# Kernel tuning notes

Hardware: AMD Instinct MI355X
Metric: run time of the kernel (lower is better)

## Reference

```python
import jax, jax.numpy as jnp
import numpy as np

H = 128  # GRU units


def _gru_dir(x, W, U, b, reverse):
    """Keras GRU (reset_after=True, gate order z,r,h). x: [B,T,D].
    Returns (final_state [B,H], all_states [B,T,H])."""
    b_i, b_h = b[0], b[1]  # input bias, recurrent bias, each [3H]
    # Precompute input projections for all timesteps: [T,B,3H]
    xp = jnp.einsum('btd,dh->tbh', x, W) + b_i

    def step(h, xt):
        rec = h @ U + b_h                       # [B,3H]
        xz, xr, xh = jnp.split(xt, 3, axis=-1)
        rz, rr, rh = jnp.split(rec, 3, axis=-1)
        z = jax.nn.sigmoid(xz + rz)
        r = jax.nn.sigmoid(xr + rr)
        hh = jnp.tanh(xh + r * rh)
        hn = z * h + (1.0 - z) * hh
        return hn, hn

    h0 = jnp.zeros((x.shape[0], H), x.dtype)
    hT, hs = jax.lax.scan(step, h0, xp, reverse=reverse)
    return hT, jnp.transpose(hs, (1, 0, 2))  # [B,T,H]


def _forward(x, Ws, Us, bs, Wd, bd):
    out = x
    for l in range(3):
        fT, f = _gru_dir(out, Ws[l, 0], Us[l, 0], bs[l, 0], reverse=False)
        bT, b = _gru_dir(out, Ws[l, 1], Us[l, 1], bs[l, 1], reverse=True)
        if l < 2:  # return_sequences=True, concat merge
            out = jnp.concatenate([f, b], axis=-1)      # [B,T,2H]
        else:      # return_sequences=False: final states
            out = jnp.concatenate([fT, bT], axis=-1)    # [B,2H]
    return jax.nn.sigmoid(out @ Wd + bd)                # [B,1]


def setup_inputs() -> dict:
    key = jax.random.key(0)
    ks = jax.random.split(key, 5)
    B, T, D = 256, 512, 256
    x = jax.random.normal(ks[0], (B, T, D), jnp.float32)
    # glorot-ish scaling to keep gates in a sane range
    Ws = jax.random.normal(ks[1], (3, 2, D, 3 * H), jnp.float32) * (1.0 / np.sqrt(D))
    Us = jax.random.normal(ks[2], (3, 2, H, 3 * H), jnp.float32) * (1.0 / np.sqrt(H))
    bs = jnp.zeros((3, 2, 2, 3 * H), jnp.float32)
    Wd = jax.random.normal(ks[3], (2 * H, 1), jnp.float32) * (1.0 / np.sqrt(2 * H))
    bd = jnp.zeros((1,), jnp.float32)
    return {"x": x, "Ws": Ws, "Us": Us, "bs": bs, "Wd": Wd, "bd": bd}


def reference(x, Ws, Us, bs, Wd, bd):
    return _forward(x, Ws, Us, bs, Wd, bd)
```

## Files before the change

kernel.cpp:

```cpp
#include <hip/hip_runtime.h>
#include <hip/hip_bf16.h>

#define DEV __device__ __forceinline__

constexpr int B_ = 256;
constexpr int T_ = 512;
constexpr int H_ = 128;
constexpr int K_ = 256;
constexpr int G_ = 384;
constexpr int M_ = B_ * T_;

using bf16 = __hip_bfloat16;
typedef short bf16x8 __attribute__((ext_vector_type(8)));
typedef float f32x4 __attribute__((ext_vector_type(4)));
typedef float f32x2 __attribute__((ext_vector_type(2)));

DEV float tof(float x) { return x; }
DEV float tof(bf16 x) { return __bfloat162float(x); }
DEV void stor(float* p, float v) { *p = v; }
DEV void stor(bf16* p, float v) { *p = __float2bfloat16(v); }

DEV unsigned short f2bs(float f) {
  union { float f; unsigned u; } v;
  v.f = f;
  unsigned r = (v.u + 0x7FFFu + ((v.u >> 16) & 1u)) >> 16;
  return (unsigned short)r;
}
DEV float bs2f(unsigned short s) {
  union { unsigned u; float f; } v;
  v.u = ((unsigned)s) << 16;
  return v.f;
}

DEV float fsigmoid(float x) {
  return __builtin_amdgcn_rcpf(1.f + __expf(-x));
}
DEV float ftanh(float x) {
  x = fminf(20.f, fmaxf(-20.f, x));
  float e = __expf(-2.f * x);
  return (1.f - e) * __builtin_amdgcn_rcpf(1.f + e);
}

DEV void barrier_lds() {
  asm volatile("s_waitcnt lgkmcnt(0)\n\ts_barrier" ::: "memory");
}

DEV void pin4(float4& v) {
  asm volatile("" : "+v"(v.x), "+v"(v.y), "+v"(v.z), "+v"(v.w));
}

DEV f32x4 mfma16(bf16x8 a, bf16x8 b, f32x4 c) {
  return __builtin_amdgcn_mfma_f32_16x16x32_bf16(a, b, c, 0, 0, 0);
}

DEV void gload16(const ushort* g, ushort* l) {
  __builtin_amdgcn_global_load_lds(
      (const __attribute__((address_space(1))) void*)g,
      (__attribute__((address_space(3))) void*)l, 16, 0, 0);
}

DEV float dppx1(float x) {
  return __int_as_float(
      __builtin_amdgcn_update_dpp(0, __float_as_int(x), 0xB1, 0xF, 0xF, true));
}
DEV float dppx2(float x) {
  return __int_as_float(
      __builtin_amdgcn_update_dpp(0, __float_as_int(x), 0x4E, 0xF, 0xF, true));
}
DEV float dppx7(float x) {
  return __int_as_float(
      __builtin_amdgcn_update_dpp(0, __float_as_int(x), 0x141, 0xF, 0xF, true));
}

__global__ __launch_bounds__(256) void convX_kernel(
    const float* __restrict__ x, ushort* __restrict__ hiA,
    ushort* __restrict__ loA) {
  const int n4 = M_ * K_ / 4;
  for (int idx = blockIdx.x * blockDim.x + threadIdx.x; idx < n4;
       idx += gridDim.x * blockDim.x) {
    float4 v = ((const float4*)x)[idx];
    ushort4 h, l;
    h.x = f2bs(v.x); l.x = f2bs(v.x - bs2f(h.x));
    h.y = f2bs(v.y); l.y = f2bs(v.y - bs2f(h.y));
    h.z = f2bs(v.z); l.z = f2bs(v.z - bs2f(h.z));
    h.w = f2bs(v.w); l.w = f2bs(v.w - bs2f(h.w));
    ((ushort4*)hiA)[idx] = h;
    ((ushort4*)loA)[idx] = l;
  }
}

__global__ __launch_bounds__(256) void convW_kernel(
    const float* __restrict__ W, ushort* __restrict__ WhiT,
    ushort* __restrict__ WloT) {
  const int ncol = blockIdx.x;
  const int dir = ncol / G_, j = ncol % G_;
  const int k = threadIdx.x;
  const float f = W[((size_t)dir * K_ + k) * G_ + j];
  const unsigned short hi = f2bs(f);
  WhiT[(size_t)ncol * K_ + k] = hi;
  WloT[(size_t)ncol * K_ + k] = f2bs(f - bs2f(hi));
}

template <typename XT>
__global__ __launch_bounds__(256, 2) void gemm3_kernel(
    const ushort* __restrict__ Ahi, const ushort* __restrict__ Alo,
    const ushort* __restrict__ WhiT, const ushort* __restrict__ WloT,
    const float* __restrict__ bbias, XT* __restrict__ xp) {
  const int m0 = blockIdx.x * 128;
  const int n0 = blockIdx.y * 128;
  const int tid = threadIdx.x;
  const int w = tid >> 6, lane = tid & 63;
  const int wm = w >> 1, wn = w & 1;
  const int col = lane & 15, quad = lane >> 4;

  __shared__ __align__(16) ushort AH[128 * 64];
  __shared__ __align__(16) ushort AL[128 * 64];
  __shared__ __align__(16) ushort BH[128 * 64];
  __shared__ __align__(16) ushort BL[128 * 64];

  f32x4 acc[4][4];
#pragma unroll
  for (int i = 0; i < 4; ++i)
#pragma unroll
    for (int n = 0; n < 4; ++n) acc[i][n] = (f32x4){0.f, 0.f, 0.f, 0.f};

  const ushort* gsrc = (w == 0) ? Ahi : (w == 1) ? Alo : (w == 2) ? WhiT : WloT;
  ushort* lds = (w == 0) ? AH : (w == 1) ? AL : (w == 2) ? BH : BL;
  const int rbase = (w < 2) ? m0 : n0;

  const int srow = lane >> 3;
  const int sl = lane & 7;

  for (int kb = 0; kb < K_; kb += 64) {
#pragma unroll
    for (int q = 0; q < 16; ++q) {
      const int r = q * 8 + srow;
      const int sc = sl ^ (r & 7);
      gload16(gsrc + (size_t)(rbase + r) * K_ + kb + sc * 8, lds + q * 512);
    }
    __syncthreads();
#pragma unroll
    for (int z = 0; z < 2; ++z) {
      const int qk = z * 4 + quad;
      bf16x8 ah[4], al[4], bh[4], bl[4];
#pragma unroll
      for (int i = 0; i < 4; ++i) {
        const int row = wm * 64 + i * 16 + col;
        const int off = row * 64 + ((qk ^ (row & 7)) << 3);
        ah[i] = *(const bf16x8*)&AH[off];
        al[i] = *(const bf16x8*)&AL[off];
      }
#pragma unroll
      for (int n = 0; n < 4; ++n) {
        const int row = wn * 64 + n * 16 + col;
        const int off = row * 64 + ((qk ^ (row & 7)) << 3);
        bh[n] = *(const bf16x8*)&BH[off];
        bl[n] = *(const bf16x8*)&BL[off];
      }
#pragma unroll
      for (int i = 0; i < 4; ++i)
#pragma unroll
        for (int n = 0; n < 4; ++n) {
          acc[i][n] = mfma16(ah[i], bh[n], acc[i][n]);
          acc[i][n] = mfma16(al[i], bh[n], acc[i][n]);
          acc[i][n] = mfma16(ah[i], bl[n], acc[i][n]);
        }
    }
    __syncthreads();
  }

  const int dir = (n0 >= G_) ? 1 : 0;
#pragma unroll
  for (int n = 0; n < 4; ++n) {
    const int ncol = n0 + wn * 64 + n * 16 + col;
    const int g = ncol - dir * G_;
    const float bv = bbias[dir * 2 * G_ + g];
#pragma unroll
    for (int i = 0; i < 4; ++i) {
      const int mb = m0 + wm * 64 + i * 16 + quad * 4;
#pragma unroll
      for (int r = 0; r < 4; ++r) {
        const int m = mb + r;
        const int bb = m >> 9;
        const int t = m & (T_ - 1);
        stor(xp + ((size_t)(dir * T_ + t) * B_ + bb) * G_ + g,
             acc[i][n][r] + bv);
      }
    }
  }
}

DEV float4 ldU4(const float* U, int col, int k0) {
  float4 v;
  v.x = U[(size_t)(k0 + 0) * G_ + col];
  v.y = U[(size_t)(k0 + 1) * G_ + col];
  v.z = U[(size_t)(k0 + 2) * G_ + col];
  v.w = U[(size_t)(k0 + 3) * G_ + col];
  return v;
}

template <typename XT, bool LAST>
__global__ __attribute__((amdgpu_flat_work_group_size(768, 768),
                          amdgpu_waves_per_eu(3, 3))) void rec_kernel(
    const XT* __restrict__ xp, const float* __restrict__ Ubase,
    const float* __restrict__ bbase, ushort* __restrict__ seqH,
    ushort* __restrict__ seqL, float* __restrict__ fin) {
  const int dir = blockIdx.y;
  const float* U = Ubase + dir * (H_ * G_);
  const float* bh = bbase + dir * (2 * G_) + G_;
  const int b0 = blockIdx.x * 2;
  const int tid = threadIdx.x;
  const int kc = tid & 7;
  const int cg = tid >> 3;
  const int kc4 = kc * 4;

  const int g = ((kc & 1) ? 4 : 0) ^ ((kc & 2) ? 2 : 0) ^ ((kc & 4) ? 7 : 0);
  const int glo = g & 3;
  const int gb2 = g >> 2;

  __shared__ __align__(16) float hbuf[2][H_];
  __shared__ float rec_s[2][G_];

#define LDU(m, i) ldU4(U, cg * 4 + ((m) ^ glo), (i) * 32 + kc4)
  float4 u00 = LDU(0, 0), u01 = LDU(0, 1), u02 = LDU(0, 2), u03 = LDU(0, 3);
  float4 u10 = LDU(1, 0), u11 = LDU(1, 1), u12 = LDU(1, 2), u13 = LDU(1, 3);
  float4 u20 = LDU(2, 0), u21 = LDU(2, 1), u22 = LDU(2, 2), u23 = LDU(2, 3);
  float4 u30 = LDU(3, 0), u31 = LDU(3, 1), u32 = LDU(3, 2), u33 = LDU(3, 3);
#undef LDU
  pin4(u00); pin4(u01); pin4(u02); pin4(u03);
  pin4(u10); pin4(u11); pin4(u12); pin4(u13);
  pin4(u20); pin4(u21); pin4(u22); pin4(u23);
  pin4(u30); pin4(u31); pin4(u32); pin4(u33);

  const float bmine = bh[cg * 4 + glo];

  const float* hA = hbuf[gb2];
  const float* hB = hbuf[gb2 ^ 1];

  const int grow = tid >> 7;
  const int gu = tid & (H_ - 1);
  const bool gateT = tid < 2 * H_;

  if (gateT) hbuf[grow][gu] = 0.f;

  const XT* xbase = xp + (size_t)(dir * T_) * B_ * G_;

  XT xzc{}, xrc{}, xhc{};
  {
    const int t0 = dir ? (T_ - 1) : 0;
    if (gateT) {
      const XT* xr_ = xbase + ((size_t)t0 * B_ + b0 + grow) * G_ + gu;
      xzc = xr_[0];
      xrc = xr_[H_];
      xhc = xr_[2 * H_];
    }
  }
  barrier_lds();

  for (int it = 0; it < T_; ++it) {
    const int t = dir ? (T_ - 1 - it) : it;

    XT xzn = xzc, xrn = xrc, xhn = xhc;
    if (gateT && (it + 1 < T_)) {
      const int tn = dir ? (t - 1) : (t + 1);
      const XT* xr_ = xbase + ((size_t)tn * B_ + b0 + grow) * G_ + gu;
      xzn = xr_[0];
      xrn = xr_[H_];
      xhn = xr_[2 * H_];
    }

    f32x2 a00 = {0.f, 0.f}, a01 = {0.f, 0.f}, a02 = {0.f, 0.f}, a03 = {0.f, 0.f};
    f32x2 a10 = {0.f, 0.f}, a11 = {0.f, 0.f}, a12 = {0.f, 0.f}, a13 = {0.f, 0.f};
#define FMA2(acc, h4, u4)                                              \
  {                                                                    \
    const f32x2* hp_ = (const f32x2*)&(h4);                            \
    const f32x2* up_ = (const f32x2*)&(u4);                            \
    acc = __builtin_elementwise_fma(hp_[0], up_[0], acc);              \
    acc = __builtin_elementwise_fma(hp_[1], up_[1], acc);              \
  }
#define DOT_I(i, uA, uB, uC, uD)                                       \
  {                                                                    \
    float4 h0 = *(const float4*)&hA[(i) * 32 + kc4];                   \
    float4 h1 = *(const float4*)&hB[(i) * 32 + kc4];                   \
    FMA2(a00, h0, uA) FMA2(a01, h0, uB) FMA2(a02, h0, uC)              \
    FMA2(a03, h0, uD)                                                  \
    FMA2(a10, h1, uA) FMA2(a11, h1, uB) FMA2(a12, h1, uC)              \
    FMA2(a13, h1, uD)                                                  \
  }
    DOT_I(0, u00, u10, u20, u30)
    DOT_I(1, u01, u11, u21, u31)
    DOT_I(2, u02, u12, u22, u32)
    DOT_I(3, u03, u13, u23, u33)
#undef DOT_I
#undef FMA2

    const float s0 = a00.x + a00.y, s1 = a01.x + a01.y;
    const float s2 = a02.x + a02.y, s3 = a03.x + a03.y;
    const float s4 = a10.x + a10.y, s5 = a11.x + a11.y;
    const float s6 = a12.x + a12.y, s7 = a13.x + a13.y;

    const float r0 = s0 + dppx1(s4);
    const float r1 = s1 + dppx1(s5);
    const float r2 = s2 + dppx1(s6);
    const float r3 = s3 + dppx1(s7);
    const float t0v = r0 + dppx2(r2);
    const float t1v = r1 + dppx2(r3);
    const float v = t0v + dppx7(t1v);

    rec_s[gb2][cg * 4 + glo] = v + bmine;
    barrier_lds();

    if (gateT) {
      const float xz = tof(xzc);
      const float xr = tof(xrc);
      const float xh = tof(xhc);
      const float rz = rec_s[grow][gu];
      const float rr = rec_s[grow][H_ + gu];
      const float rh = rec_s[grow][2 * H_ + gu];
      const float z = fsigmoid(xz + rz);
      const float r = fsigmoid(xr + rr);
      const float hh = ftanh(xh + r * rh);
      const float hold = hbuf[grow][gu];
      const float hn = z * hold + (1.f - z) * hh;
      hbuf[grow][gu] = hn;
      if constexpr (!LAST) {
        const size_t sidx =
            ((size_t)(b0 + grow) * T_ + t) * (2 * H_) + dir * H_ + gu;
        const unsigned short hi = f2bs(hn);
        seqH[sidx] = hi;
        seqL[sidx] = f2bs(hn - bs2f(hi));
      }
      xzc = xzn;
      xrc = xrn;
      xhc = xhn;
    }
    barrier_lds();
  }

  if constexpr (LAST) {
    if (gateT) fin[(size_t)(b0 + grow) * (2 * H_) + dir * H_ + gu] =
        hbuf[grow][gu];
  }
}

__global__ void dense_kernel(const float* __restrict__ fin,
                             const float* __restrict__ Wd,
                             const float* __restrict__ bd,
                             float* __restrict__ out) {
  __shared__ float w[2 * H_];
  const int tid = threadIdx.x;
  w[tid] = Wd[tid];
  __syncthreads();
  float s = bd[0];
  const float* row = fin + tid * (2 * H_);
#pragma unroll 8
  for (int jj = 0; jj < 2 * H_; ++jj) s = fmaf(row[jj], w[jj], s);
  out[tid] = 1.f / (1.f + __expf(-s));
}

template <typename XT>
static void run_model(const float* x, const float* Ws, const float* Us,
                      const float* bs, const float* Wd, const float* bd,
                      float* out, char* ws, hipStream_t stream) {
  const size_t xpB = (size_t)2 * T_ * B_ * G_ * sizeof(XT);
  const size_t seqB = (size_t)B_ * T_ * 2 * H_ * 2;
  XT* xp = (XT*)ws;
  ushort* sHA = (ushort*)(ws + xpB);
  ushort* sLA = (ushort*)(ws + xpB + seqB);
  ushort* sHB = (ushort*)(ws + xpB + 2 * seqB);
  ushort* sLB = (ushort*)(ws + xpB + 3 * seqB);
  ushort* WhiT = (ushort*)(ws + xpB + 4 * seqB);
  ushort* WloT = WhiT + (size_t)768 * K_;
  float* fin = (float*)(ws + xpB + 4 * seqB + (size_t)2 * 768 * K_ * 2);

  convX_kernel<<<4096, 256, 0, stream>>>(x, sHB, sLB);

  const ushort* AHs[3] = {sHB, sHA, sHB};
  const ushort* ALs[3] = {sLB, sLA, sLB};
  ushort* oH[3] = {sHA, sHB, nullptr};
  ushort* oL[3] = {sLA, sLB, nullptr};

  for (int l = 0; l < 3; ++l) {
    const float* Wl = Ws + (size_t)l * 2 * K_ * G_;
    const float* bl = bs + (size_t)l * 4 * G_;
    const float* Ul = Us + (size_t)l * 2 * H_ * G_;
    convW_kernel<<<768, 256, 0, stream>>>(Wl, WhiT, WloT);
    gemm3_kernel<XT><<<dim3(M_ / 128, 6), 256, 0, stream>>>(
        AHs[l], ALs[l], WhiT, WloT, bl, xp);
    if (l < 2)
      rec_kernel<XT, false><<<dim3(B_ / 2, 2), 768, 0, stream>>>(
          xp, Ul, bl, oH[l], oL[l], nullptr);
    else
      rec_kernel<XT, true><<<dim3(B_ / 2, 2), 768, 0, stream>>>(
          xp, Ul, bl, nullptr, nullptr, fin);
  }
  dense_kernel<<<1, B_, 0, stream>>>(fin, Wd, bd, out);
}

extern "C" void kernel_launch(void* const* d_in, const int* in_sizes, int n_in,
                              void* d_out, int out_size, void* d_ws,
                              size_t ws_size, hipStream_t stream) {
  const float* x = (const float*)d_in[0];
  const float* Ws = (const float*)d_in[1];
  const float* Us = (const float*)d_in[2];
  const float* bs = (const float*)d_in[3];
  const float* Wd = (const float*)d_in[4];
  const float* bd = (const float*)d_in[5];
  float* out = (float*)d_out;
  char* ws = (char*)d_ws;

  const size_t seqB = (size_t)B_ * T_ * 2 * H_ * 2;
  const size_t wtB = (size_t)2 * 768 * K_ * 2;
  const size_t finB = (size_t)B_ * 2 * H_ * 4;
  const size_t xp32 = (size_t)2 * T_ * B_ * G_ * 4;
  const size_t tierA = xp32 + 4 * seqB + wtB + finB;
  if (ws_size >= tierA)
    run_model<float>(x, Ws, Us, bs, Wd, bd, out, ws, stream);
  else
    run_model<bf16>(x, Ws, Us, bs, Wd, bd, out, ws, stream);
}
```

Baseline: 2.173 ms.

## Process one batch row per recurrent block and double block count

```diff
diff --git a/kernel.cpp b/kernel.cpp
--- a/kernel.cpp
+++ b/kernel.cpp
@@ -201,27 +201,25 @@
 
 template <typename XT, bool LAST>
 __global__ __attribute__((amdgpu_flat_work_group_size(768, 768),
-                          amdgpu_waves_per_eu(3, 3))) void rec_kernel(
+                          amdgpu_waves_per_eu(6))) void rec_kernel(
     const XT* __restrict__ xp, const float* __restrict__ Ubase,
     const float* __restrict__ bbase, ushort* __restrict__ seqH,
     ushort* __restrict__ seqL, float* __restrict__ fin) {
   const int dir = blockIdx.y;
+  const int b = blockIdx.x;
   const float* U = Ubase + dir * (H_ * G_);
   const float* bh = bbase + dir * (2 * G_) + G_;
-  const int b0 = blockIdx.x * 2;
   const int tid = threadIdx.x;
   const int kc = tid & 7;
   const int cg = tid >> 3;
   const int kc4 = kc * 4;
 
-  const int g = ((kc & 1) ? 4 : 0) ^ ((kc & 2) ? 2 : 0) ^ ((kc & 4) ? 7 : 0);
-  const int glo = g & 3;
-  const int gb2 = g >> 2;
-
-  __shared__ __align__(16) float hbuf[2][H_];
-  __shared__ float rec_s[2][G_];
-
-#define LDU(m, i) ldU4(U, cg * 4 + ((m) ^ glo), (i) * 32 + kc4)
+  const int g = ((kc & 1) ? 2 : 0) ^ ((kc & 4) ? 3 : 0);
+
+  __shared__ __align__(16) float hbuf[H_];
+  __shared__ float rec_s[G_];
+
+#define LDU(m, i) ldU4(U, cg * 4 + ((m) ^ g), (i) * 32 + kc4)
   float4 u00 = LDU(0, 0), u01 = LDU(0, 1), u02 = LDU(0, 2), u03 = LDU(0, 3);
   float4 u10 = LDU(1, 0), u11 = LDU(1, 1), u12 = LDU(1, 2), u13 = LDU(1, 3);
   float4 u20 = LDU(2, 0), u21 = LDU(2, 1), u22 = LDU(2, 2), u23 = LDU(2, 3);
@@ -232,16 +230,12 @@
   pin4(u20); pin4(u21); pin4(u22); pin4(u23);
   pin4(u30); pin4(u31); pin4(u32); pin4(u33);
 
-  const float bmine = bh[cg * 4 + glo];
-
-  const float* hA = hbuf[gb2];
-  const float* hB = hbuf[gb2 ^ 1];
-
-  const int grow = tid >> 7;
-  const int gu = tid & (H_ - 1);
-  const bool gateT = tid < 2 * H_;
-
-  if (gateT) hbuf[grow][gu] = 0.f;
+  const float bmine = bh[cg * 4 + g];
+
+  const int gu = tid;
+  const bool gateT = tid < H_;
+
+  if (gateT) hbuf[gu] = 0.f;
 
   const XT* xbase = xp + (size_t)(dir * T_) * B_ * G_;
 
@@ -249,12 +243,13 @@
   {
     const int t0 = dir ? (T_ - 1) : 0;
     if (gateT) {
-      const XT* xr_ = xbase + ((size_t)t0 * B_ + b0 + grow) * G_ + gu;
+      const XT* xr_ = xbase + ((size_t)t0 * B_ + b) * G_ + gu;
       xzc = xr_[0];
       xrc = xr_[H_];
       xhc = xr_[2 * H_];
     }
   }
+  float hprev = 0.f;
   barrier_lds();
 
   for (int it = 0; it < T_; ++it) {
@@ -263,14 +258,13 @@
     XT xzn = xzc, xrn = xrc, xhn = xhc;
     if (gateT && (it + 1 < T_)) {
       const int tn = dir ? (t - 1) : (t + 1);
-      const XT* xr_ = xbase + ((size_t)tn * B_ + b0 + grow) * G_ + gu;
+      const XT* xr_ = xbase + ((size_t)tn * B_ + b) * G_ + gu;
       xzn = xr_[0];
       xrn = xr_[H_];
       xhn = xr_[2 * H_];
     }
 
-    f32x2 a00 = {0.f, 0.f}, a01 = {0.f, 0.f}, a02 = {0.f, 0.f}, a03 = {0.f, 0.f};
-    f32x2 a10 = {0.f, 0.f}, a11 = {0.f, 0.f}, a12 = {0.f, 0.f}, a13 = {0.f, 0.f};
+    f32x2 a0 = {0.f, 0.f}, a1 = {0.f, 0.f}, a2 = {0.f, 0.f}, a3 = {0.f, 0.f};
 #define FMA2(acc, h4, u4)                                              \
   {                                                                    \
     const f32x2* hp_ = (const f32x2*)&(h4);                            \
@@ -280,12 +274,8 @@
   }
 #define DOT_I(i, uA, uB, uC, uD)                                       \
   {                                                                    \
-    float4 h0 = *(const float4*)&hA[(i) * 32 + kc4];                   \
-    float4 h1 = *(const float4*)&hB[(i) * 32 + kc4];                   \
-    FMA2(a00, h0, uA) FMA2(a01, h0, uB) FMA2(a02, h0, uC)              \
-    FMA2(a03, h0, uD)                                                  \
-    FMA2(a10, h1, uA) FMA2(a11, h1, uB) FMA2(a12, h1, uC)              \
-    FMA2(a13, h1, uD)                                                  \
+    float4 h0 = *(const float4*)&hbuf[(i) * 32 + kc4];                 \
+    FMA2(a0, h0, uA) FMA2(a1, h0, uB) FMA2(a2, h0, uC) FMA2(a3, h0, uD)\
   }
     DOT_I(0, u00, u10, u20, u30)
     DOT_I(1, u01, u11, u21, u31)
@@ -294,38 +284,34 @@
 #undef DOT_I
 #undef FMA2
 
-    const float s0 = a00.x + a00.y, s1 = a01.x + a01.y;
-    const float s2 = a02.x + a02.y, s3 = a03.x + a03.y;
-    const float s4 = a10.x + a10.y, s5 = a11.x + a11.y;
-    const float s6 = a12.x + a12.y, s7 = a13.x + a13.y;
-
-    const float r0 = s0 + dppx1(s4);
-    const float r1 = s1 + dppx1(s5);
-    const float r2 = s2 + dppx1(s6);
-    const float r3 = s3 + dppx1(s7);
-    const float t0v = r0 + dppx2(r2);
-    const float t1v = r1 + dppx2(r3);
-    const float v = t0v + dppx7(t1v);
-
-    rec_s[gb2][cg * 4 + glo] = v + bmine;
+    const float s0 = a0.x + a0.y;
+    const float s1 = a1.x + a1.y;
+    const float s2 = a2.x + a2.y;
+    const float s3 = a3.x + a3.y;
+
+    const float r0 = s0 + dppx1(s2);
+    const float r1 = s1 + dppx1(s3);
+    const float t0v = r0 + dppx7(r1);
+    const float v = t0v + dppx2(t0v);
+
+    if ((kc & 2) == 0) rec_s[cg * 4 + g] = v + bmine;
     barrier_lds();
 
     if (gateT) {
       const float xz = tof(xzc);
       const float xr = tof(xrc);
       const float xh = tof(xhc);
-      const float rz = rec_s[grow][gu];
-      const float rr = rec_s[grow][H_ + gu];
-      const float rh = rec_s[grow][2 * H_ + gu];
+      const float rz = rec_s[gu];
+      const float rr = rec_s[H_ + gu];
+      const float rh = rec_s[2 * H_ + gu];
       const float z = fsigmoid(xz + rz);
       const float r = fsigmoid(xr + rr);
       const float hh = ftanh(xh + r * rh);
-      const float hold = hbuf[grow][gu];
-      const float hn = z * hold + (1.f - z) * hh;
-      hbuf[grow][gu] = hn;
+      const float hn = z * hprev + (1.f - z) * hh;
+      hprev = hn;
+      hbuf[gu] = hn;
       if constexpr (!LAST) {
-        const size_t sidx =
-            ((size_t)(b0 + grow) * T_ + t) * (2 * H_) + dir * H_ + gu;
+        const size_t sidx = ((size_t)b * T_ + t) * (2 * H_) + dir * H_ + gu;
         const unsigned short hi = f2bs(hn);
         seqH[sidx] = hi;
         seqL[sidx] = f2bs(hn - bs2f(hi));
@@ -338,8 +324,7 @@
   }
 
   if constexpr (LAST) {
-    if (gateT) fin[(size_t)(b0 + grow) * (2 * H_) + dir * H_ + gu] =
-        hbuf[grow][gu];
+    if (gateT) fin[(size_t)b * (2 * H_) + dir * H_ + gu] = hprev;
   }
 }
 
@@ -388,10 +373,10 @@
     gemm3_kernel<XT><<<dim3(M_ / 128, 6), 256, 0, stream>>>(
         AHs[l], ALs[l], WhiT, WloT, bl, xp);
     if (l < 2)
-      rec_kernel<XT, false><<<dim3(B_ / 2, 2), 768, 0, stream>>>(
+      rec_kernel<XT, false><<<dim3(B_, 2), 768, 0, stream>>>(
           xp, Ul, bl, oH[l], oL[l], nullptr);
     else
-      rec_kernel<XT, true><<<dim3(B_ / 2, 2), 768, 0, stream>>>(
+      rec_kernel<XT, true><<<dim3(B_, 2), 768, 0, stream>>>(
           xp, Ul, bl, nullptr, nullptr, fin);
   }
   dense_kernel<<<1, B_, 0, stream>>>(fin, Wd, bd, out);
```

Result: slower. 4.854 ms (+123.3%).
